# Optimization experiments

Measured on AMD Instinct MI355X. Metric: run time of the kernel, lower is better.

The kernel has to match this reference:

```python
import jax, jax.numpy as jnp
import numpy as np

H = 768
NH = 12
HD = H // NH

def _layernorm(x, g, b, eps=1e-5):
    mu = jnp.mean(x, axis=-1, keepdims=True)
    var = jnp.var(x, axis=-1, keepdims=True)
    return (x - mu) * jax.lax.rsqrt(var + eps) * g + b

def setup_inputs() -> dict:
    key = jax.random.key(0)
    ks = jax.random.split(key, 16)
    s = 0.02
    inp = {
        "x": jax.random.normal(ks[0], (2, 2048, H), jnp.float32),
        "t": jax.random.normal(ks[1], (2, 1, H), jnp.float32),
        # MHA params
        "w_qkv": jax.random.normal(ks[2], (H, 3 * H), jnp.float32) * s,
        "b_qkv": jnp.zeros((3 * H,), jnp.float32),
        "w_mffn1": jax.random.normal(ks[3], (H, 4 * H), jnp.float32) * s,
        "b_mffn1": jnp.zeros((4 * H,), jnp.float32),
        "w_mffn2": jax.random.normal(ks[4], (4 * H, H), jnp.float32) * s,
        "b_mffn2": jnp.zeros((H,), jnp.float32),
        # scale_shift (adaLN) params
        "w_ss1": jax.random.normal(ks[5], (H, 6 * H), jnp.float32) * s,
        "b_ss1": jnp.zeros((6 * H,), jnp.float32),
        "w_ss2": jax.random.normal(ks[6], (6 * H, 6 * H), jnp.float32) * s,
        "b_ss2": jnp.zeros((6 * H,), jnp.float32),
        # layernorms
        "ln1_g": jnp.ones((H,), jnp.float32),
        "ln1_b": jnp.zeros((H,), jnp.float32),
        "ln2_g": jnp.ones((H,), jnp.float32),
        "ln2_b": jnp.zeros((H,), jnp.float32),
        # DiT block FFN
        "w_ffn1": jax.random.normal(ks[7], (H, 4 * H), jnp.float32) * s,
        "b_ffn1": jnp.zeros((4 * H,), jnp.float32),
        "w_ffn2": jax.random.normal(ks[8], (4 * H, H), jnp.float32) * s,
        "b_ffn2": jnp.zeros((H,), jnp.float32),
    }
    return inp

def _mha(x, w_qkv, b_qkv, w1, b1, w2, b2):
    B, T, _ = x.shape
    qkv = x @ w_qkv + b_qkv                      # [B,T,3H]
    qkv = qkv.reshape(B, T, 3, NH, HD)           # split (n h s) as in rearrange
    q, k, v = [jnp.transpose(qkv[:, :, i], (0, 2, 1, 3)) for i in range(3)]  # [B,NH,T,HD]
    # NOTE: faithful to source: scale by 1/sqrt(hidden_size), not head_dim
    wei = jnp.einsum('bhtd,bhsd->bhts', q, k) / jnp.sqrt(jnp.asarray(H, x.dtype))
    wei = jax.nn.softmax(wei, axis=-1)           # [B,NH,T,T] (dropout p=0)
    o = jnp.einsum('bhts,bhsd->bhtd', wei, v)    # [B,NH,T,HD]
    o = jnp.transpose(o, (0, 2, 1, 3)).reshape(B, T, H)
    o = jax.nn.gelu(o @ w1 + b1, approximate=False) @ w2 + b2
    return o

def reference(x, t, w_qkv, b_qkv, w_mffn1, b_mffn1, w_mffn2, b_mffn2,
              w_ss1, b_ss1, w_ss2, b_ss2, ln1_g, ln1_b, ln2_g, ln2_b,
              w_ffn1, b_ffn1, w_ffn2, b_ffn2):
    t_emb = jax.nn.silu(t @ w_ss1 + b_ss1) @ w_ss2 + b_ss2   # [B,1,6H]
    g1, be1, a1, g2, be2, a2 = jnp.split(t_emb, 6, axis=-1)  # each [B,1,H]
    residual = x
    h = g1 * _layernorm(x, ln1_g, ln1_b) + be1
    h = _mha(h, w_qkv, b_qkv, w_mffn1, b_mffn1, w_mffn2, b_mffn2)
    x = residual + a1 * h
    residual = x
    h = g2 * _layernorm(x, ln2_g, ln2_b) + be2
    h = jax.nn.gelu(h @ w_ffn1 + b_ffn1, approximate=False) @ w_ffn2 + b_ffn2
    x = residual + a2 * h
    return x
```

## Files before the change

### kernel.cpp

```cpp
#include <hip/hip_runtime.h>
#include <hip/hip_bf16.h>
#include <cstdint>

typedef __bf16 bf16x8 __attribute__((ext_vector_type(8)));
typedef float f32x4 __attribute__((ext_vector_type(4)));
typedef float f32x16 __attribute__((ext_vector_type(16)));

#define SCALE_Q_LOG2E 0.052058770734702875f

__device__ inline float fast_exp2(float x) { return __builtin_amdgcn_exp2f(x); }

struct PrepArgs {
  const float* src[5];
  __hip_bfloat16* dst[5];
  int K[5], N[5];
  int start[6];
  const float* tin;
  const float* w_ss1;
  float* tacc1;
};

__global__ __launch_bounds__(256) void k_prep(PrepArgs pa) {
  __shared__ float tile[64][65];
  int bid = blockIdx.x;
  int tid = threadIdx.x;
  if (bid < pa.start[5]) {
    int i = 0;
#pragma unroll
    for (int j = 1; j < 5; ++j)
      if (bid >= pa.start[j]) i = j;
    int t0 = bid - pa.start[i];
    int N = pa.N[i], K = pa.K[i];
    int ntx = N >> 6;
    int bx = t0 % ntx, by = t0 / ntx;
    const float* src = pa.src[i];
    __hip_bfloat16* dst = pa.dst[i];
    int n0 = bx * 64, k0 = by * 64;
    int c4 = tid & 15, rr = tid >> 4;
    float4 v[4];
#pragma unroll
    for (int p = 0; p < 4; ++p)
      v[p] = *(const float4*)&src[(size_t)(k0 + rr + 16 * p) * N + n0 + c4 * 4];
#pragma unroll
    for (int p = 0; p < 4; ++p) {
      tile[rr + 16 * p][c4 * 4 + 0] = v[p].x;
      tile[rr + 16 * p][c4 * 4 + 1] = v[p].y;
      tile[rr + 16 * p][c4 * 4 + 2] = v[p].z;
      tile[rr + 16 * p][c4 * 4 + 3] = v[p].w;
    }
    __syncthreads();
    int kg = tid & 15, nl = tid >> 4;
#pragma unroll
    for (int p = 0; p < 4; ++p) {
      int n = nl + 16 * p;
      __hip_bfloat16 t4[4];
#pragma unroll
      for (int j = 0; j < 4; ++j) t4[j] = __float2bfloat16(tile[kg * 4 + j][n]);
      *(uint2*)&dst[(size_t)(n0 + n) * K + k0 + kg * 4] = *(uint2*)t4;
    }
  } else {
    int t0 = bid - pa.start[5];
    int nb = t0 % 18, kb0 = (t0 / 18) * 16;
    int n = nb * 256 + tid;
    float wv[16];
#pragma unroll
    for (int kk = 0; kk < 16; ++kk)
      wv[kk] = pa.w_ss1[(size_t)(kb0 + kk) * 4608 + n];
    float a0 = 0.f, a1 = 0.f;
#pragma unroll
    for (int kk = 0; kk < 16; ++kk) {
      a0 += pa.tin[kb0 + kk] * wv[kk];
      a1 += pa.tin[768 + kb0 + kk] * wv[kk];
    }
    atomicAdd(&pa.tacc1[n], a0);
    atomicAdd(&pa.tacc1[4608 + n], a1);
  }
}

__global__ void k_tvec2_silu(const float* __restrict__ tacc1, const float* __restrict__ bss1,
                             const float* __restrict__ W, float* __restrict__ teacc) {
  int n2 = blockIdx.x * 256 + threadIdx.x;
  int kb = blockIdx.y * 64;
  float a0x = 0.f, a0y = 0.f, a1x = 0.f, a1y = 0.f;
#pragma unroll 1
  for (int kc = 0; kc < 4; ++kc) {
    int k0 = kb + kc * 16;
    float2 wv[16];
#pragma unroll
    for (int kk = 0; kk < 16; ++kk)
      wv[kk] = *(const float2*)&W[(size_t)(k0 + kk) * 4608 + n2 * 2];
#pragma unroll
    for (int kk = 0; kk < 16; ++kk) {
      int k = k0 + kk;
      float bs = bss1[k];
      float t0 = tacc1[k] + bs;
      float t1 = tacc1[4608 + k] + bs;
      t0 = t0 / (1.f + expf(-t0));
      t1 = t1 / (1.f + expf(-t1));
      a0x += t0 * wv[kk].x; a0y += t0 * wv[kk].y;
      a1x += t1 * wv[kk].x; a1y += t1 * wv[kk].y;
    }
  }
  atomicAdd(&teacc[n2 * 2 + 0], a0x);
  atomicAdd(&teacc[n2 * 2 + 1], a0y);
  atomicAdd(&teacc[4608 + n2 * 2 + 0], a1x);
  atomicAdd(&teacc[4608 + n2 * 2 + 1], a1y);
}

__global__ void k_ln_mod(const float* __restrict__ x, const float* __restrict__ lng,
                         const float* __restrict__ lnb, const float* __restrict__ teacc,
                         const float* __restrict__ bss2,
                         int gofs, int bofs, __hip_bfloat16* __restrict__ out) {
  int row = blockIdx.x;
  int b = row >> 11;
  const float* xr = x + (size_t)row * 768;
  int tid = threadIdx.x;
  float v[3];
  float s = 0.f, sq = 0.f;
#pragma unroll
  for (int i = 0; i < 3; ++i) { v[i] = xr[tid + 256 * i]; s += v[i]; sq += v[i] * v[i]; }
#pragma unroll
  for (int o = 32; o > 0; o >>= 1) { s += __shfl_xor(s, o); sq += __shfl_xor(sq, o); }
  __shared__ float rs[4], rq[4];
  int w = tid >> 6, lane = tid & 63;
  if (lane == 0) { rs[w] = s; rq[w] = sq; }
  __syncthreads();
  s = rs[0] + rs[1] + rs[2] + rs[3];
  sq = rq[0] + rq[1] + rq[2] + rq[3];
  float mu = s * (1.f / 768.f);
  float var = sq * (1.f / 768.f) - mu * mu;
  float rstd = rsqrtf(var + 1e-5f);
  const float* tb = teacc + (size_t)b * 4608;
#pragma unroll
  for (int i = 0; i < 3; ++i) {
    int n = tid + 256 * i;
    float gv = tb[gofs + n] + bss2[gofs + n];
    float bv = tb[bofs + n] + bss2[bofs + n];
    float h = (v[i] - mu) * rstd * lng[n] + lnb[n];
    h = gv * h + bv;
    out[(size_t)row * 768 + n] = __float2bfloat16(h);
  }
}

template <int BM, int BN, int EPI>
__global__ __launch_bounds__(256)
void k_gemm(const __hip_bfloat16* __restrict__ A,
            const __hip_bfloat16* __restrict__ Bt,
            const float* __restrict__ bias,
            float* __restrict__ outF, __hip_bfloat16* __restrict__ outB,
            __hip_bfloat16* __restrict__ outV,
            const float* __restrict__ res, const float* __restrict__ teacc,
            const float* __restrict__ bss2,
            int gofs, int M, int N, int K) {
  constexpr int MI = BM / 32;
  constexpr int NI = BN / 32;
  __shared__ __align__(16) __hip_bfloat16 As[BM * 64];
  __shared__ __align__(16) __hip_bfloat16 Bs[BN * 64];
  const int tid = threadIdx.x;
  const int w = tid >> 6, lane = tid & 63;
  const int quad = lane >> 4, l16 = lane & 15;
  const int wm = w & 1, wn = w >> 1;
  const int m0 = blockIdx.y * BM, n0 = blockIdx.x * BN;
  const int srow = lane >> 3;
  const int sco = ((lane & 7) ^ srow) * 8;

  f32x4 acc[MI][NI] = {};

  for (int k0 = 0; k0 < K; k0 += 64) {
#pragma unroll
    for (int ii = 0; ii < BM / 32; ++ii) {
      int is = w * (BM / 32) + ii;
      const __hip_bfloat16* g = A + (size_t)(m0 + is * 8 + srow) * K + k0 + sco;
      __builtin_amdgcn_global_load_lds(
          (const __attribute__((address_space(1))) void*)g,
          (__attribute__((address_space(3))) void*)&As[is * 512], 16, 0, 0);
    }
#pragma unroll
    for (int ii = 0; ii < BN / 32; ++ii) {
      int is = w * (BN / 32) + ii;
      const __hip_bfloat16* g = Bt + (size_t)(n0 + is * 8 + srow) * K + k0 + sco;
      __builtin_amdgcn_global_load_lds(
          (const __attribute__((address_space(1))) void*)g,
          (__attribute__((address_space(3))) void*)&Bs[is * 512], 16, 0, 0);
    }
    __syncthreads();
#pragma unroll
    for (int ks = 0; ks < 2; ++ks) {
      bf16x8 af[MI], bfv[NI];
#pragma unroll
      for (int i = 0; i < MI; ++i) {
        int row = wm * (BM / 2) + i * 16 + l16;
        int cph = (ks * 4 + quad) ^ (row & 7);
        af[i] = *(const bf16x8*)&As[row * 64 + cph * 8];
      }
#pragma unroll
      for (int j = 0; j < NI; ++j) {
        int row = wn * (BN / 2) + j * 16 + l16;
        int cph = (ks * 4 + quad) ^ (row & 7);
        bfv[j] = *(const bf16x8*)&Bs[row * 64 + cph * 8];
      }
#pragma unroll
      for (int i = 0; i < MI; ++i)
#pragma unroll
        for (int j = 0; j < NI; ++j)
          acc[i][j] = __builtin_amdgcn_mfma_f32_16x16x32_bf16(af[i], bfv[j], acc[i][j], 0, 0, 0);
    }
    __syncthreads();
  }

#pragma unroll
  for (int j = 0; j < NI; ++j) {
    int col = n0 + wn * (BN / 2) + j * 16 + l16;
    float bs = bias[col];
#pragma unroll
    for (int i = 0; i < MI; ++i) {
      int row0 = m0 + wm * (BM / 2) + i * 16 + quad * 4;
      if (EPI == 3 && col >= 1536) {
        int d = col - 1536;
        int nh = d >> 6, dl = d & 63;
        int bb = row0 >> 11, tok = row0 & 2047;
        __hip_bfloat16 tmp[4];
#pragma unroll
        for (int r = 0; r < 4; ++r) tmp[r] = __float2bfloat16(acc[i][j][r] + bs);
        *(uint2*)&outV[((size_t)(bb * 12 + nh) * 64 + dl) * 2048 + tok] = *(uint2*)tmp;
      } else {
#pragma unroll
        for (int r = 0; r < 4; ++r) {
          int row = row0 + r;
          float v = acc[i][j][r] + bs;
          size_t idx = (size_t)row * N + col;
          if (EPI == 0) {
            outF[idx] = v;
          } else if (EPI == 1) {
            float v2 = v * v;
            float u = v * (0.79788456080286536f + 0.035677408136300125f * v2);
            float e = fast_exp2(u * 2.8853900817779268f);
            float gl = v - v * __builtin_amdgcn_rcpf(e + 1.f);
            outB[idx] = __float2bfloat16(gl);
          } else if (EPI == 2) {
            float gate = teacc[(size_t)(row >> 11) * 4608 + gofs + col] + bss2[gofs + col];
            outF[idx] = res[idx] + gate * v;
          } else {
            float vq = (col < 768) ? v * SCALE_Q_LOG2E : v;
            outB[idx] = __float2bfloat16(vq);
          }
        }
      }
    }
  }
}

__launch_bounds__(256)
__global__ void k_attn(const __hip_bfloat16* __restrict__ qkvb,
                       const __hip_bfloat16* __restrict__ VT,
                       float* __restrict__ Opart,
                       float* __restrict__ lpart) {
  __shared__ __align__(16) __hip_bfloat16 Ks[128 * 64];
  __shared__ __align__(16) __hip_bfloat16 Vs[64 * 128];

  const int tid = threadIdx.x;
  const int w = tid >> 6, lane = tid & 63;
  const int l32 = lane & 31, hi = lane >> 5;
  const int qt = blockIdx.x, nh = blockIdx.y;
  const int b = blockIdx.z >> 1, half = blockIdx.z & 1;
  const int bh = b * 12 + nh;

  const int qrow0 = b * 2048 + qt * 128 + w * 32;
  bf16x8 qf[4];
#pragma unroll
  for (int dg = 0; dg < 4; ++dg)
    qf[dg] = *(const bf16x8*)(qkvb + (size_t)(qrow0 + l32) * 2304 + nh * 64 + dg * 16 + hi * 8);

  f32x16 o0 = {}, o1 = {};
  float lsum = 0.f;

  const int krow = lane >> 3;
  const int kco = ((lane & 7) ^ krow) * 8;

  for (int kt = 0; kt < 8; ++kt) {
    const int tok0 = b * 2048 + half * 1024 + kt * 128;
    __syncthreads();
#pragma unroll
    for (int ii = 0; ii < 4; ++ii) {
      int i = w * 4 + ii;
      const __hip_bfloat16* gk =
          qkvb + (size_t)(tok0 + i * 8 + krow) * 2304 + 768 + nh * 64 + kco;
      __builtin_amdgcn_global_load_lds(
          (const __attribute__((address_space(1))) void*)gk,
          (__attribute__((address_space(3))) void*)&Ks[i * 512], 16, 0, 0);
      int vd = i * 4 + (lane >> 4);
      const __hip_bfloat16* gv =
          VT + (size_t)(bh * 64 + vd) * 2048 + half * 1024 + kt * 128 +
          (((lane & 15) ^ (vd & 15)) * 8);
      __builtin_amdgcn_global_load_lds(
          (const __attribute__((address_space(1))) void*)gv,
          (__attribute__((address_space(3))) void*)&Vs[i * 512], 16, 0, 0);
    }
    __syncthreads();

#pragma unroll
    for (int g2 = 0; g2 < 4; ++g2) {
      f32x16 s = {};
      __builtin_amdgcn_s_setprio(1);
#pragma unroll
      for (int dg = 0; dg < 4; ++dg) {
        int tok = g2 * 32 + l32;
        int phys = (dg * 2 + hi) ^ (tok & 7);
        bf16x8 kf = *(const bf16x8*)&Ks[tok * 64 + phys * 8];
        s = __builtin_amdgcn_mfma_f32_32x32x16_bf16(kf, qf[dg], s, 0, 0, 0);
      }
      __builtin_amdgcn_s_setprio(0);

      float p[16];
#pragma unroll
      for (int r = 0; r < 16; ++r) { p[r] = fast_exp2(s[r]); lsum += p[r]; }
      uint32_t wd[8];
#pragma unroll
      for (int i2 = 0; i2 < 8; ++i2)
        asm("v_cvt_pk_bf16_f32 %0, %1, %2" : "=v"(wd[i2]) : "v"(p[2 * i2]), "v"(p[2 * i2 + 1]));
      asm("v_permlane32_swap_b32 %0, %1" : "+v"(wd[0]), "+v"(wd[2]));
      asm("v_permlane32_swap_b32 %0, %1" : "+v"(wd[1]), "+v"(wd[3]));
      asm("v_permlane32_swap_b32 %0, %1" : "+v"(wd[4]), "+v"(wd[6]));
      asm("v_permlane32_swap_b32 %0, %1" : "+v"(wd[5]), "+v"(wd[7]));

      __builtin_amdgcn_s_setprio(1);
#pragma unroll
      for (int s01 = 0; s01 < 2; ++s01) {
        union { uint32_t u[4]; bf16x8 v; } fr;
        fr.u[0] = wd[s01 * 4 + 0]; fr.u[1] = wd[s01 * 4 + 1];
        fr.u[2] = wd[s01 * 4 + 2]; fr.u[3] = wd[s01 * 4 + 3];
        int ks = g2 * 2 + s01;
#pragma unroll
        for (int dh = 0; dh < 2; ++dh) {
          int row = dh * 32 + l32;
          int phys = (ks * 2 + hi) ^ (row & 15);
          bf16x8 vf = *(const bf16x8*)&Vs[row * 128 + phys * 8];
          if (dh == 0) o0 = __builtin_amdgcn_mfma_f32_32x32x16_bf16(fr.v, vf, o0, 0, 0, 0);
          else         o1 = __builtin_amdgcn_mfma_f32_32x32x16_bf16(fr.v, vf, o1, 0, 0, 0);
        }
      }
      __builtin_amdgcn_s_setprio(0);
    }
  }

  lsum += __shfl_xor(lsum, 32);
  {
    float* op = Opart + (size_t)half * 4096 * 768;
#pragma unroll
    for (int r = 0; r < 16; ++r) {
      int q = (r & 3) + 8 * (r >> 2) + 4 * hi;
      size_t rowofs = (size_t)(qrow0 + q) * 768 + nh * 64;
      op[rowofs + l32]      = o0[r];
      op[rowofs + 32 + l32] = o1[r];
    }
    if (lane < 32)
      lpart[((size_t)half * 4096 + qrow0 + l32) * 12 + nh] = lsum;
  }
}

__global__ __launch_bounds__(192)
void k_attn_comb(const float* __restrict__ Opart, const float* __restrict__ lpart,
                 __hip_bfloat16* __restrict__ out) {
  int row = blockIdx.x;
  int tid = threadIdx.x;
  int c0 = tid * 4;
  int nh = c0 >> 6;
  float l = lpart[((size_t)row) * 12 + nh] + lpart[((size_t)4096 + row) * 12 + nh];
  float inv = 1.f / l;
  const float* o0 = Opart + (size_t)row * 768 + c0;
  const float* o1 = Opart + (size_t)(4096 + row) * 768 + c0;
  float4 a = *(const float4*)o0;
  float4 bq = *(const float4*)o1;
  __hip_bfloat16 t4[4];
  t4[0] = __float2bfloat16((a.x + bq.x) * inv);
  t4[1] = __float2bfloat16((a.y + bq.y) * inv);
  t4[2] = __float2bfloat16((a.z + bq.z) * inv);
  t4[3] = __float2bfloat16((a.w + bq.w) * inv);
  *(uint2*)&out[(size_t)row * 768 + c0] = *(uint2*)t4;
}

extern "C" void kernel_launch(void* const* d_in, const int* in_sizes, int n_in,
                              void* d_out, int out_size, void* d_ws, size_t ws_size,
                              hipStream_t stream) {
  const float* x      = (const float*)d_in[0];
  const float* t      = (const float*)d_in[1];
  const float* w_qkv  = (const float*)d_in[2];
  const float* b_qkv  = (const float*)d_in[3];
  const float* w_m1   = (const float*)d_in[4];
  const float* b_m1   = (const float*)d_in[5];
  const float* w_m2   = (const float*)d_in[6];
  const float* b_m2   = (const float*)d_in[7];
  const float* w_ss1  = (const float*)d_in[8];
  const float* b_ss1  = (const float*)d_in[9];
  const float* w_ss2  = (const float*)d_in[10];
  const float* b_ss2  = (const float*)d_in[11];
  const float* ln1_g  = (const float*)d_in[12];
  const float* ln1_b  = (const float*)d_in[13];
  const float* ln2_g  = (const float*)d_in[14];
  const float* ln2_b  = (const float*)d_in[15];
  const float* w_f1   = (const float*)d_in[16];
  const float* b_f1   = (const float*)d_in[17];
  const float* w_f2   = (const float*)d_in[18];
  const float* b_f2   = (const float*)d_in[19];
  float* out = (float*)d_out;

  char* ws = (char*)d_ws;
  size_t off = 0;
  auto alloc = [&](size_t bytes) -> char* {
    off = (off + 255) & ~(size_t)255;
    char* p = ws + off;
    off += bytes;
    return p;
  };
  __hip_bfloat16* wtq  = (__hip_bfloat16*)alloc((size_t)2304 * 768 * 2);
  __hip_bfloat16* wtm1 = (__hip_bfloat16*)alloc((size_t)3072 * 768 * 2);
  __hip_bfloat16* wtm2 = (__hip_bfloat16*)alloc((size_t)768 * 3072 * 2);
  __hip_bfloat16* wtf1 = (__hip_bfloat16*)alloc((size_t)3072 * 768 * 2);
  __hip_bfloat16* wtf2 = (__hip_bfloat16*)alloc((size_t)768 * 3072 * 2);
  float* tacc1 = (float*)alloc(9216 * 4);
  float* teacc = (float*)alloc(9216 * 4);
  __hip_bfloat16* h1   = (__hip_bfloat16*)alloc((size_t)4096 * 768 * 2);
  __hip_bfloat16* qkvb = (__hip_bfloat16*)alloc((size_t)4096 * 2304 * 2);
  __hip_bfloat16* VT   = (__hip_bfloat16*)alloc((size_t)24 * 64 * 2048 * 2);
  __hip_bfloat16* attn = (__hip_bfloat16*)alloc((size_t)4096 * 768 * 2);
  __hip_bfloat16* act1 = (__hip_bfloat16*)alloc((size_t)4096 * 3072 * 2);
  float* x1            = (float*)alloc((size_t)4096 * 768 * 4);
  float* Opart         = (float*)alloc((size_t)2 * 4096 * 768 * 4);
  float* lpart         = (float*)alloc((size_t)2 * 4096 * 12 * 4);

  (void)hipMemsetAsync(tacc1, 0, 9216 * 4, stream);
  (void)hipMemsetAsync(teacc, 0, 9216 * 4, stream);

  PrepArgs pa;
  pa.src[0] = w_qkv; pa.dst[0] = wtq;  pa.K[0] = 768;  pa.N[0] = 2304;
  pa.src[1] = w_m1;  pa.dst[1] = wtm1; pa.K[1] = 768;  pa.N[1] = 3072;
  pa.src[2] = w_m2;  pa.dst[2] = wtm2; pa.K[2] = 3072; pa.N[2] = 768;
  pa.src[3] = w_f1;  pa.dst[3] = wtf1; pa.K[3] = 768;  pa.N[3] = 3072;
  pa.src[4] = w_f2;  pa.dst[4] = wtf2; pa.K[4] = 3072; pa.N[4] = 768;
  pa.start[0] = 0;
  pa.start[1] = pa.start[0] + (2304 / 64) * (768 / 64);
  pa.start[2] = pa.start[1] + (3072 / 64) * (768 / 64);
  pa.start[3] = pa.start[2] + (768 / 64) * (3072 / 64);
  pa.start[4] = pa.start[3] + (3072 / 64) * (768 / 64);
  pa.start[5] = pa.start[4] + (768 / 64) * (3072 / 64);
  pa.tin = t; pa.w_ss1 = w_ss1; pa.tacc1 = tacc1;
  int tvec1_blocks = 18 * 48;
  k_prep<<<pa.start[5] + tvec1_blocks, 256, 0, stream>>>(pa);

  k_tvec2_silu<<<dim3(4608 / 512, 4608 / 64), 256, 0, stream>>>(tacc1, b_ss1, w_ss2, teacc);

  k_ln_mod<<<4096, 256, 0, stream>>>(x, ln1_g, ln1_b, teacc, b_ss2, 0, 768, h1);
  k_gemm<64, 128, 3><<<dim3(2304 / 128, 4096 / 64), 256, 0, stream>>>(
      h1, wtq, b_qkv, nullptr, qkvb, VT, nullptr, nullptr, nullptr, 0, 4096, 2304, 768);
  k_attn<<<dim3(16, 12, 4), 256, 0, stream>>>(qkvb, VT, Opart, lpart);
  k_attn_comb<<<4096, 192, 0, stream>>>(Opart, lpart, attn);
  k_gemm<128, 128, 1><<<dim3(3072 / 128, 4096 / 128), 256, 0, stream>>>(
      attn, wtm1, b_m1, nullptr, act1, nullptr, nullptr, nullptr, nullptr, 0, 4096, 3072, 768);
  k_gemm<64, 64, 2><<<dim3(768 / 64, 4096 / 64), 256, 0, stream>>>(
      act1, wtm2, b_m2, x1, nullptr, nullptr, x, teacc, b_ss2, 1536, 4096, 768, 3072);

  k_ln_mod<<<4096, 256, 0, stream>>>(x1, ln2_g, ln2_b, teacc, b_ss2, 2304, 3072, h1);
  k_gemm<128, 128, 1><<<dim3(3072 / 128, 4096 / 128), 256, 0, stream>>>(
      h1, wtf1, b_f1, nullptr, act1, nullptr, nullptr, nullptr, nullptr, 0, 4096, 3072, 768);
  k_gemm<64, 64, 2><<<dim3(768 / 64, 4096 / 64), 256, 0, stream>>>(
      act1, wtf2, b_f2, out, nullptr, nullptr, x1, teacc, b_ss2, 3840, 4096, 768, 3072);
}
```

Before: 427.2 us.

## Add block swizzle, K=128 down-projection GEMM kernel, and bf16 attention partials

Remaps GEMM block indices so consecutive blocks are spread across eight groups, aiming for better cache locality. Adds a dedicated down-projection kernel (k_gemm2) that stages K=128 per iteration with 16x16x32 MFMAs for the residual-gated epilogue, halving the number of loop iterations and barriers. Stores the split-KV attention partial outputs in bf16 instead of fp32, halving write and read traffic in the combine step at some precision cost. The swizzle assumes the block count divides by eight.

```diff
diff --git a/kernel.cpp b/kernel.cpp
--- a/kernel.cpp
+++ b/kernel.cpp
@@ -160,7 +160,11 @@
   const int w = tid >> 6, lane = tid & 63;
   const int quad = lane >> 4, l16 = lane & 15;
   const int wm = w & 1, wn = w >> 1;
-  const int m0 = blockIdx.y * BM, n0 = blockIdx.x * BN;
+  const int nx = gridDim.x;
+  const int lin = blockIdx.y * nx + blockIdx.x;
+  const int cpx = (nx * gridDim.y) >> 3;
+  const int sw = (lin & 7) * cpx + (lin >> 3);
+  const int m0 = (sw / nx) * BM, n0 = (sw % nx) * BN;
   const int srow = lane >> 3;
   const int sco = ((lane & 7) ^ srow) * 8;
 
@@ -237,9 +241,6 @@
             float e = fast_exp2(u * 2.8853900817779268f);
             float gl = v - v * __builtin_amdgcn_rcpf(e + 1.f);
             outB[idx] = __float2bfloat16(gl);
-          } else if (EPI == 2) {
-            float gate = teacc[(size_t)(row >> 11) * 4608 + gofs + col] + bss2[gofs + col];
-            outF[idx] = res[idx] + gate * v;
           } else {
             float vq = (col < 768) ? v * SCALE_Q_LOG2E : v;
             outB[idx] = __float2bfloat16(vq);
@@ -250,10 +251,92 @@
   }
 }
 
+__global__ __launch_bounds__(256)
+void k_gemm2(const __hip_bfloat16* __restrict__ A,
+             const __hip_bfloat16* __restrict__ Bt,
+             const float* __restrict__ bias,
+             float* __restrict__ outF,
+             const float* __restrict__ res, const float* __restrict__ teacc,
+             const float* __restrict__ bss2,
+             int gofs, int M, int N, int K) {
+  __shared__ __align__(16) __hip_bfloat16 As[64 * 128];
+  __shared__ __align__(16) __hip_bfloat16 Bs[64 * 128];
+  const int tid = threadIdx.x;
+  const int w = tid >> 6, lane = tid & 63;
+  const int quad = lane >> 4, l16 = lane & 15;
+  const int wm = w & 1, wn = w >> 1;
+  const int nx = gridDim.x;
+  const int lin = blockIdx.y * nx + blockIdx.x;
+  const int cpx = (nx * gridDim.y) >> 3;
+  const int sw = (lin & 7) * cpx + (lin >> 3);
+  const int m0 = (sw / nx) * 64, n0 = (sw % nx) * 64;
+  const int srow4 = lane >> 4;
+
+  f32x4 acc[2][2] = {};
+
+  for (int k0 = 0; k0 < K; k0 += 128) {
+#pragma unroll
+    for (int ii = 0; ii < 4; ++ii) {
+      int i = w * 4 + ii;
+      int row = i * 4 + srow4;
+      int sc = ((lane & 15) ^ (row & 15)) * 8;
+      const __hip_bfloat16* gA = A + (size_t)(m0 + row) * K + k0 + sc;
+      __builtin_amdgcn_global_load_lds(
+          (const __attribute__((address_space(1))) void*)gA,
+          (__attribute__((address_space(3))) void*)&As[i * 512], 16, 0, 0);
+      const __hip_bfloat16* gB = Bt + (size_t)(n0 + row) * K + k0 + sc;
+      __builtin_amdgcn_global_load_lds(
+          (const __attribute__((address_space(1))) void*)gB,
+          (__attribute__((address_space(3))) void*)&Bs[i * 512], 16, 0, 0);
+    }
+    __syncthreads();
+#pragma unroll
+    for (int ks = 0; ks < 4; ++ks) {
+      bf16x8 af[2], bfv[2];
+#pragma unroll
+      for (int i = 0; i < 2; ++i) {
+        int row = wm * 32 + i * 16 + l16;
+        int phys = (ks * 4 + quad) ^ (row & 15);
+        af[i] = *(const bf16x8*)&As[row * 128 + phys * 8];
+      }
+#pragma unroll
+      for (int j = 0; j < 2; ++j) {
+        int row = wn * 32 + j * 16 + l16;
+        int phys = (ks * 4 + quad) ^ (row & 15);
+        bfv[j] = *(const bf16x8*)&Bs[row * 128 + phys * 8];
+      }
+#pragma unroll
+      for (int i = 0; i < 2; ++i)
+#pragma unroll
+        for (int j = 0; j < 2; ++j)
+          acc[i][j] = __builtin_amdgcn_mfma_f32_16x16x32_bf16(af[i], bfv[j], acc[i][j], 0, 0, 0);
+    }
+    __syncthreads();
+  }
+
+#pragma unroll
+  for (int j = 0; j < 2; ++j) {
+    int col = n0 + wn * 32 + j * 16 + l16;
+    float bs = bias[col];
+#pragma unroll
+    for (int i = 0; i < 2; ++i) {
+      int row0 = m0 + wm * 32 + i * 16 + quad * 4;
+#pragma unroll
+      for (int r = 0; r < 4; ++r) {
+        int row = row0 + r;
+        float v = acc[i][j][r] + bs;
+        size_t idx = (size_t)row * N + col;
+        float gate = teacc[(size_t)(row >> 11) * 4608 + gofs + col] + bss2[gofs + col];
+        outF[idx] = res[idx] + gate * v;
+      }
+    }
+  }
+}
+
 __launch_bounds__(256)
 __global__ void k_attn(const __hip_bfloat16* __restrict__ qkvb,
                        const __hip_bfloat16* __restrict__ VT,
-                       float* __restrict__ Opart,
+                       __hip_bfloat16* __restrict__ Opart,
                        float* __restrict__ lpart) {
   __shared__ __align__(16) __hip_bfloat16 Ks[128 * 64];
   __shared__ __align__(16) __hip_bfloat16 Vs[64 * 128];
@@ -345,13 +428,13 @@
 
   lsum += __shfl_xor(lsum, 32);
   {
-    float* op = Opart + (size_t)half * 4096 * 768;
+    __hip_bfloat16* op = Opart + (size_t)half * 4096 * 768;
 #pragma unroll
     for (int r = 0; r < 16; ++r) {
       int q = (r & 3) + 8 * (r >> 2) + 4 * hi;
       size_t rowofs = (size_t)(qrow0 + q) * 768 + nh * 64;
-      op[rowofs + l32]      = o0[r];
-      op[rowofs + 32 + l32] = o1[r];
+      op[rowofs + l32]      = __float2bfloat16(o0[r]);
+      op[rowofs + 32 + l32] = __float2bfloat16(o1[r]);
     }
     if (lane < 32)
       lpart[((size_t)half * 4096 + qrow0 + l32) * 12 + nh] = lsum;
@@ -359,7 +442,7 @@
 }
 
 __global__ __launch_bounds__(192)
-void k_attn_comb(const float* __restrict__ Opart, const float* __restrict__ lpart,
+void k_attn_comb(const __hip_bfloat16* __restrict__ Opart, const float* __restrict__ lpart,
                  __hip_bfloat16* __restrict__ out) {
   int row = blockIdx.x;
   int tid = threadIdx.x;
@@ -367,15 +450,14 @@
   int nh = c0 >> 6;
   float l = lpart[((size_t)row) * 12 + nh] + lpart[((size_t)4096 + row) * 12 + nh];
   float inv = 1.f / l;
-  const float* o0 = Opart + (size_t)row * 768 + c0;
-  const float* o1 = Opart + (size_t)(4096 + row) * 768 + c0;
-  float4 a = *(const float4*)o0;
-  float4 bq = *(const float4*)o1;
+  uint2 u0 = *(const uint2*)&Opart[(size_t)row * 768 + c0];
+  uint2 u1 = *(const uint2*)&Opart[(size_t)(4096 + row) * 768 + c0];
+  const __hip_bfloat16* p0 = (const __hip_bfloat16*)&u0;
+  const __hip_bfloat16* p1 = (const __hip_bfloat16*)&u1;
   __hip_bfloat16 t4[4];
-  t4[0] = __float2bfloat16((a.x + bq.x) * inv);
-  t4[1] = __float2bfloat16((a.y + bq.y) * inv);
-  t4[2] = __float2bfloat16((a.z + bq.z) * inv);
-  t4[3] = __float2bfloat16((a.w + bq.w) * inv);
+#pragma unroll
+  for (int j = 0; j < 4; ++j)
+    t4[j] = __float2bfloat16((__bfloat162float(p0[j]) + __bfloat162float(p1[j])) * inv);
   *(uint2*)&out[(size_t)row * 768 + c0] = *(uint2*)t4;
 }
 
@@ -425,7 +507,7 @@
   __hip_bfloat16* attn = (__hip_bfloat16*)alloc((size_t)4096 * 768 * 2);
   __hip_bfloat16* act1 = (__hip_bfloat16*)alloc((size_t)4096 * 3072 * 2);
   float* x1            = (float*)alloc((size_t)4096 * 768 * 4);
-  float* Opart         = (float*)alloc((size_t)2 * 4096 * 768 * 4);
+  __hip_bfloat16* Opart = (__hip_bfloat16*)alloc((size_t)2 * 4096 * 768 * 2);
   float* lpart         = (float*)alloc((size_t)2 * 4096 * 12 * 4);
 
   (void)hipMemsetAsync(tacc1, 0, 9216 * 4, stream);
@@ -456,12 +538,12 @@
   k_attn_comb<<<4096, 192, 0, stream>>>(Opart, lpart, attn);
   k_gemm<128, 128, 1><<<dim3(3072 / 128, 4096 / 128), 256, 0, stream>>>(
       attn, wtm1, b_m1, nullptr, act1, nullptr, nullptr, nullptr, nullptr, 0, 4096, 3072, 768);
-  k_gemm<64, 64, 2><<<dim3(768 / 64, 4096 / 64), 256, 0, stream>>>(
-      act1, wtm2, b_m2, x1, nullptr, nullptr, x, teacc, b_ss2, 1536, 4096, 768, 3072);
+  k_gemm2<<<dim3(768 / 64, 4096 / 64), 256, 0, stream>>>(
+      act1, wtm2, b_m2, x1, x, teacc, b_ss2, 1536, 4096, 768, 3072);
 
   k_ln_mod<<<4096, 256, 0, stream>>>(x1, ln2_g, ln2_b, teacc, b_ss2, 2304, 3072, h1);
   k_gemm<128, 128, 1><<<dim3(3072 / 128, 4096 / 128), 256, 0, stream>>>(
       h1, wtf1, b_f1, nullptr, act1, nullptr, nullptr, nullptr, nullptr, 0, 4096, 3072, 768);
-  k_gemm<64, 64, 2><<<dim3(768 / 64, 4096 / 64), 256, 0, stream>>>(
-      act1, wtf2, b_f2, out, nullptr, nullptr, x1, teacc, b_ss2, 3840, 4096, 768, 3072);
-}
+  k_gemm2<<<dim3(768 / 64, 4096 / 64), 256, 0, stream>>>(
+      act1, wtf2, b_f2, out, x1, teacc, b_ss2, 3840, 4096, 768, 3072);
+}
```

Measured after the change: 418.8 us. 2.0% less time.
